# Kernel optimization log

Hardware: AMD Instinct MI355X
Metric: run time of the kernel (lower is better)

The kernel has to match this reference:

```python
import jax, jax.numpy as jnp
import numpy as np

T, H, I, E, K = 1024, 2880, 2880, 16, 4
ALPHA = 1.702   # gemm1_alpha
LIMIT = 7.0     # swiglu_limit (gemm1_clamp_limit)


def setup_inputs() -> dict:
    key = jax.random.key(0)
    ks = jax.random.split(key, 9)
    s = 0.02  # init scale to keep activations sane
    return {
        "hidden_states": jax.random.normal(ks[0], (T, H), jnp.float32),
        "router_w": jax.random.normal(ks[1], (E, H), jnp.float32) * s,
        "router_b": jax.random.normal(ks[2], (E,), jnp.float32) * s,
        "w_gate": jax.random.normal(ks[3], (E, H, I), jnp.float32) * s,
        "b_gate": jax.random.normal(ks[4], (E, I), jnp.float32) * s,
        "w_up": jax.random.normal(ks[5], (E, H, I), jnp.float32) * s,
        "b_up": jax.random.normal(ks[6], (E, I), jnp.float32) * s,
        "w_down": jax.random.normal(ks[7], (E, I, H), jnp.float32) * s,
        "b_down": jax.random.normal(ks[8], (E, H), jnp.float32) * s,
    }


def reference(hidden_states, router_w, router_b, w_gate, b_gate, w_up, b_up, w_down, b_down):
    x = hidden_states  # [T, H]
    # Router: ReplicatedLinear(hidden_size, num_experts, bias=True)
    logits = x @ router_w.T + router_b            # [T, E]
    # TopK(top_k=K, renormalize=True): softmax -> top-k -> renormalize
    probs = jax.nn.softmax(logits, axis=-1)
    top_w, top_i = jax.lax.top_k(probs, K)        # [T, K]
    top_w = top_w / jnp.sum(top_w, axis=-1, keepdims=True)
    # combine weights scattered back to [T, E] (rows sum to 1)
    comb = jnp.sum(jax.nn.one_hot(top_i, E, dtype=x.dtype) * top_w[..., None], axis=1)
    # Expert grouped GEMM (dense over experts; combine weights zero out unused)
    g = jnp.einsum('th,ehi->eti', x, w_gate) + b_gate[:, None, :]   # [E, T, I]
    u = jnp.einsum('th,ehi->eti', x, w_up) + b_up[:, None, :]       # [E, T, I]
    # gpt-oss clamped swiglu: gate clamp max, up clamp both sides
    g = jnp.minimum(g, LIMIT)
    u = jnp.clip(u, -LIMIT, LIMIT)
    act = (u + 1.0) * (g * jax.nn.sigmoid(g * ALPHA))               # [E, T, I]
    y = jnp.einsum('eti,eih->eth', act, w_down) + b_down[:, None, :]  # [E, T, H]
    out = jnp.einsum('te,eth->th', comb, y)                          # [T, H]
    return out
```

## Files before the change

kernel.cpp:

```cpp
#include <hip/hip_runtime.h>
#include <stdint.h>

#define T_TOK 1024
#define HD 2880
#define ID 2880
#define NE 16
#define NTOP 4

#define BM 128
#define BN 64
#define BK 64
#define NKT (HD / BK)
#define NIB (ID / BN)
#define NMB (T_TOK / BM)
#define NB1 (NE * NIB * NMB)

typedef short bf16x8 __attribute__((ext_vector_type(8)));
typedef float f32x4 __attribute__((ext_vector_type(4)));

__device__ __forceinline__ uint4 pack8f(const float* v) {
    union { __bf16 b[8]; uint4 q; } p;
#pragma unroll
    for (int j = 0; j < 8; j++) p.b[j] = (__bf16)v[j];
    return p.q;
}
__device__ __forceinline__ unsigned short bf16bits(float f) {
    union { __bf16 b[2]; unsigned short u[2]; } p;
    p.b[0] = (__bf16)f;
    return p.u[0];
}

__global__ __launch_bounds__(256) void k_init(float* __restrict__ out, int* __restrict__ cnt) {
    int i = blockIdx.x * 256 + threadIdx.x;
    ((float4*)out)[i] = make_float4(0.f, 0.f, 0.f, 0.f);
    if (blockIdx.x == 0 && threadIdx.x < NE) cnt[threadIdx.x] = 0;
}

__global__ __launch_bounds__(256) void k_router(
    const float* __restrict__ x, const float* __restrict__ rw, const float* __restrict__ rb,
    float* __restrict__ topw, int* __restrict__ cnt, int* __restrict__ list)
{
    const int t = blockIdx.x;
    const int tid = threadIdx.x;
    float acc[NE];
#pragma unroll
    for (int e = 0; e < NE; e++) acc[e] = 0.f;
    for (int c = tid; c < HD; c += 256) {
        float xv = x[(size_t)t * HD + c];
#pragma unroll
        for (int e = 0; e < NE; e++) acc[e] += xv * rw[(size_t)e * HD + c];
    }
    __shared__ float red[4][NE];
    const int lane = tid & 63, wv = tid >> 6;
#pragma unroll
    for (int e = 0; e < NE; e++) {
        float v = acc[e];
#pragma unroll
        for (int off = 32; off > 0; off >>= 1) v += __shfl_down(v, off, 64);
        if (lane == 0) red[wv][e] = v;
    }
    __syncthreads();
    if (tid == 0) {
        float p[NE];
        float mx = -1e30f;
        for (int e = 0; e < NE; e++) {
            float v = red[0][e] + red[1][e] + red[2][e] + red[3][e] + rb[e];
            p[e] = v; mx = fmaxf(mx, v);
        }
        for (int e = 0; e < NE; e++) p[e] = expf(p[e] - mx);
        int sel[NTOP]; float pw[NTOP]; float ssum = 0.f;
        for (int k = 0; k < NTOP; k++) {
            float best = -1.f; int bi = 0;
            for (int e = 0; e < NE; e++)
                if (p[e] > best) { best = p[e]; bi = e; }
            sel[k] = bi; pw[k] = best; ssum += best; p[bi] = -2.f;
        }
        for (int k = 0; k < NTOP; k++) {
            topw[t * NTOP + k] = pw[k] / ssum;
            int e = sel[k];
            int pos = atomicAdd(&cnt[e], 1);
            list[e * T_TOK + pos] = t * NTOP + k;
        }
    }
}

__global__ void k_scan(const int* __restrict__ cnt, int* __restrict__ offs) {
    if (threadIdx.x == 0 && blockIdx.x == 0) {
        int s = 0;
        for (int e = 0; e < NE; e++) { offs[e] = s; s += cnt[e]; }
        offs[NE] = s;
    }
}

__global__ __launch_bounds__(512) void k_gemm1(
    const float* __restrict__ x,
    const float* __restrict__ wg, const float* __restrict__ bg,
    const float* __restrict__ wu, const float* __restrict__ bu,
    const int* __restrict__ cnt, const int* __restrict__ offs,
    const int* __restrict__ list,
    unsigned short* __restrict__ act)
{
    const int lin = blockIdx.x;
    const int logical = (lin & 7) * (NB1 / 8) + (lin >> 3);
    const int mblk = logical & 7;
    const int iblk = (logical >> 3) % NIB;
    const int e = logical / (NIB * NMB);

    const int count = cnt[e];
    const int m0 = mblk * BM;
    if (m0 >= count) return;
    const int mcount = min(BM, count - m0);
    const int i0 = iblk * BN;
    const int tid = threadIdx.x;

    __shared__ char sA[2][BM * BK * 2];
    __shared__ char sG[2][BN * BK * 2];
    __shared__ char sU[2][BN * BK * 2];
    __shared__ int lidx[BM];

    if (tid < BM) lidx[tid] = list[e * T_TOK + m0 + min(tid, mcount - 1)];
    __syncthreads();

    const int ar = tid >> 2, acg = tid & 3;
    const float* asrc = x + (size_t)(lidx[ar] >> 2) * HD + acg * 16;

    const int wtid = tid & 255;
    const int wc = wtid & 63, whg = wtid >> 6;
    const float* wsrc = (tid < 256 ? wg : wu) + ((size_t)e * HD + whg * 16) * ID + i0 + wc;
    char* const wdst0 = (tid < 256 ? sG[0] : sU[0]);
    char* const wdst1 = (tid < 256 ? sG[1] : sU[1]);

    const int lane = tid & 63, wid = tid >> 6;
    const int wm = wid >> 1, wn = wid & 1;
    const int lr = lane & 15, lk = lane >> 4;

    float4 ra[4];
    float rwv[16];

#define LOAD1(kt) do { \
        const float* s_ = asrc + (kt) * BK; \
        ra[0] = ((const float4*)s_)[0]; ra[1] = ((const float4*)s_)[1]; \
        ra[2] = ((const float4*)s_)[2]; ra[3] = ((const float4*)s_)[3]; \
        const float* w_ = wsrc + (size_t)(kt) * BK * ID; \
        _Pragma("unroll") \
        for (int j_ = 0; j_ < 16; j_++) rwv[j_] = w_[(size_t)j_ * ID]; \
    } while (0)

#define STORE1(buf) do { \
        float v_[16]; \
        _Pragma("unroll") \
        for (int p_ = 0; p_ < 4; p_++) { \
            v_[p_ * 4 + 0] = ra[p_].x; v_[p_ * 4 + 1] = ra[p_].y; \
            v_[p_ * 4 + 2] = ra[p_].z; v_[p_ * 4 + 3] = ra[p_].w; \
        } \
        *(uint4*)(sA[buf] + ar * 128 + (((acg * 2) ^ (ar & 7)) * 16)) = pack8f(v_); \
        *(uint4*)(sA[buf] + ar * 128 + (((acg * 2 + 1) ^ (ar & 7)) * 16)) = pack8f(v_ + 8); \
        char* wd_ = (buf) ? wdst1 : wdst0; \
        *(uint4*)(wd_ + wc * 128 + (((whg * 2) ^ (wc & 7)) * 16)) = pack8f(rwv); \
        *(uint4*)(wd_ + wc * 128 + (((whg * 2 + 1) ^ (wc & 7)) * 16)) = pack8f(rwv + 8); \
    } while (0)

    f32x4 accG[2][2], accU[2][2];
#pragma unroll
    for (int mb = 0; mb < 2; mb++)
#pragma unroll
        for (int cb = 0; cb < 2; cb++) {
            accG[mb][cb] = (f32x4){0.f, 0.f, 0.f, 0.f};
            accU[mb][cb] = (f32x4){0.f, 0.f, 0.f, 0.f};
        }

    LOAD1(0);
    STORE1(0);
    __syncthreads();

    for (int kt = 0; kt < NKT; kt++) {
        const int cur = kt & 1;
        const bool more = (kt + 1 < NKT);
        if (more) LOAD1(kt + 1);
        const char* cA = sA[cur];
        const char* cG = sG[cur];
        const char* cU = sU[cur];
#pragma unroll
        for (int ks = 0; ks < 2; ks++) {
            const int s = ks * 4 + lk;
            bf16x8 af[2], gf[2], uf[2];
#pragma unroll
            for (int mb = 0; mb < 2; mb++) {
                int rr = wm * 32 + mb * 16 + lr;
                af[mb] = *(const bf16x8*)(cA + rr * 128 + ((s ^ (rr & 7)) * 16));
            }
#pragma unroll
            for (int cb = 0; cb < 2; cb++) {
                int ii = wn * 32 + cb * 16 + lr;
                gf[cb] = *(const bf16x8*)(cG + ii * 128 + ((s ^ (ii & 7)) * 16));
                uf[cb] = *(const bf16x8*)(cU + ii * 128 + ((s ^ (ii & 7)) * 16));
            }
#pragma unroll
            for (int mb = 0; mb < 2; mb++)
#pragma unroll
                for (int cb = 0; cb < 2; cb++) {
                    accG[mb][cb] = __builtin_amdgcn_mfma_f32_16x16x32_bf16(af[mb], gf[cb], accG[mb][cb], 0, 0, 0);
                    accU[mb][cb] = __builtin_amdgcn_mfma_f32_16x16x32_bf16(af[mb], uf[cb], accU[mb][cb], 0, 0, 0);
                }
        }
        if (more) STORE1(cur ^ 1);
        __syncthreads();
    }
#undef LOAD1
#undef STORE1

    const int gbase = offs[e] + m0;
#pragma unroll
    for (int mb = 0; mb < 2; mb++)
#pragma unroll
        for (int cb = 0; cb < 2; cb++) {
            const int col = i0 + wn * 32 + cb * 16 + lr;
            const float bgv = bg[e * ID + col];
            const float buv = bu[e * ID + col];
#pragma unroll
            for (int q = 0; q < 4; q++) {
                const int r = wm * 32 + mb * 16 + lk * 4 + q;
                if (r < mcount) {
                    float gv = fminf(accG[mb][cb][q] + bgv, 7.0f);
                    float uv = fminf(fmaxf(accU[mb][cb][q] + buv, -7.0f), 7.0f);
                    float av = (uv + 1.0f) * (gv / (1.0f + __expf(-1.702f * gv)));
                    act[(size_t)(gbase + r) * ID + col] = bf16bits(av);
                }
            }
        }
}

__global__ __launch_bounds__(512) void k_gemm2(
    const unsigned short* __restrict__ act,
    const float* __restrict__ wd, const float* __restrict__ bd,
    const float* __restrict__ topw,
    const int* __restrict__ cnt, const int* __restrict__ offs,
    const int* __restrict__ list,
    float* __restrict__ out)
{
    const int lin = blockIdx.x;
    const int logical = (lin & 7) * (NB1 / 8) + (lin >> 3);
    const int mblk = logical & 7;
    const int hblk = (logical >> 3) % NIB;
    const int e = logical / (NIB * NMB);

    const int count = cnt[e];
    const int m0 = mblk * BM;
    if (m0 >= count) return;
    const int mcount = min(BM, count - m0);
    const int h0 = hblk * BN;
    const int tid = threadIdx.x;
    const int gbase = offs[e] + m0;

    __shared__ char sA[2][BM * BK * 2];
    __shared__ char sW[2][BN * BK * 2];
    __shared__ int lidx[BM];

    if (tid < BM) lidx[tid] = list[e * T_TOK + m0 + min(tid, mcount - 1)];
    __syncthreads();

    const int ar = tid >> 2, acg = tid & 3;
    const int arow = gbase + min(ar, mcount - 1);
    const unsigned short* asrc = act + (size_t)arow * ID + acg * 16;

    const int wc = tid & 63, whg = tid >> 6;
    const float* wsrc = wd + (size_t)e * ID * HD + (size_t)(whg * 8) * HD + h0 + wc;

    const int lane = tid & 63, wid = tid >> 6;
    const int wm = wid >> 1, wn = wid & 1;
    const int lr = lane & 15, lk = lane >> 4;

    uint4 ra0, ra1;
    float rwv[8];

#define LOAD2(kt) do { \
        const uint4* s_ = (const uint4*)(asrc + (kt) * BK); \
        ra0 = s_[0]; ra1 = s_[1]; \
        const float* w_ = wsrc + (size_t)(kt) * BK * HD; \
        _Pragma("unroll") \
        for (int j_ = 0; j_ < 8; j_++) rwv[j_] = w_[(size_t)j_ * HD]; \
    } while (0)

#define STORE2(buf) do { \
        *(uint4*)(sA[buf] + ar * 128 + (((acg * 2) ^ (ar & 7)) * 16)) = ra0; \
        *(uint4*)(sA[buf] + ar * 128 + (((acg * 2 + 1) ^ (ar & 7)) * 16)) = ra1; \
        *(uint4*)(sW[buf] + wc * 128 + ((whg ^ (wc & 7)) * 16)) = pack8f(rwv); \
    } while (0)

    f32x4 acc[2][2];
#pragma unroll
    for (int mb = 0; mb < 2; mb++)
#pragma unroll
        for (int cb = 0; cb < 2; cb++) acc[mb][cb] = (f32x4){0.f, 0.f, 0.f, 0.f};

    LOAD2(0);
    STORE2(0);
    __syncthreads();

    for (int kt = 0; kt < NKT; kt++) {
        const int cur = kt & 1;
        const bool more = (kt + 1 < NKT);
        if (more) LOAD2(kt + 1);
        const char* cA = sA[cur];
        const char* cW = sW[cur];
#pragma unroll
        for (int ks = 0; ks < 2; ks++) {
            const int s = ks * 4 + lk;
            bf16x8 af[2], wf[2];
#pragma unroll
            for (int mb = 0; mb < 2; mb++) {
                int rr = wm * 32 + mb * 16 + lr;
                af[mb] = *(const bf16x8*)(cA + rr * 128 + ((s ^ (rr & 7)) * 16));
            }
#pragma unroll
            for (int cb = 0; cb < 2; cb++) {
                int ii = wn * 32 + cb * 16 + lr;
                wf[cb] = *(const bf16x8*)(cW + ii * 128 + ((s ^ (ii & 7)) * 16));
            }
#pragma unroll
            for (int mb = 0; mb < 2; mb++)
#pragma unroll
                for (int cb = 0; cb < 2; cb++)
                    acc[mb][cb] = __builtin_amdgcn_mfma_f32_16x16x32_bf16(af[mb], wf[cb], acc[mb][cb], 0, 0, 0);
        }
        if (more) STORE2(cur ^ 1);
        __syncthreads();
    }
#undef LOAD2
#undef STORE2

#pragma unroll
    for (int mb = 0; mb < 2; mb++)
#pragma unroll
        for (int cb = 0; cb < 2; cb++) {
            const int col = h0 + wn * 32 + cb * 16 + lr;
            const float bdv = bd[e * HD + col];
#pragma unroll
            for (int q = 0; q < 4; q++) {
                const int r = wm * 32 + mb * 16 + lk * 4 + q;
                if (r < mcount) {
                    int idx = lidx[r];
                    float w = topw[idx];
                    atomicAdd(&out[(size_t)(idx >> 2) * HD + col], w * (acc[mb][cb][q] + bdv));
                }
            }
        }
}

extern "C" void kernel_launch(void* const* d_in, const int* in_sizes, int n_in,
                              void* d_out, int out_size, void* d_ws, size_t ws_size,
                              hipStream_t stream)
{
    const float* x  = (const float*)d_in[0];
    const float* rw = (const float*)d_in[1];
    const float* rb = (const float*)d_in[2];
    const float* wg = (const float*)d_in[3];
    const float* bg = (const float*)d_in[4];
    const float* wu = (const float*)d_in[5];
    const float* bu = (const float*)d_in[6];
    const float* wd = (const float*)d_in[7];
    const float* bd = (const float*)d_in[8];
    float* out = (float*)d_out;

    char* ws = (char*)d_ws;
    int*   cnt  = (int*)(ws + 0);
    int*   offs = (int*)(ws + 256);
    float* topw = (float*)(ws + 1024);
    int*   list = (int*)(ws + 32768);
    unsigned short* act = (unsigned short*)(ws + 131072);

    hipLaunchKernelGGL(k_init, dim3(T_TOK * HD / 1024), dim3(256), 0, stream, out, cnt);
    hipLaunchKernelGGL(k_router, dim3(T_TOK), dim3(256), 0, stream, x, rw, rb, topw, cnt, list);
    hipLaunchKernelGGL(k_scan, dim3(1), dim3(64), 0, stream, cnt, offs);
    hipLaunchKernelGGL(k_gemm1, dim3(NB1), dim3(512), 0, stream,
                       x, wg, bg, wu, bu, cnt, offs, list, act);
    hipLaunchKernelGGL(k_gemm2, dim3(NB1), dim3(512), 0, stream,
                       act, wd, bd, topw, cnt, offs, list, out);
}
```

Before: 1.082 ms.

## Pre-convert x to bf16 and load A fragments directly from global memory

```diff
diff --git a/kernel.cpp b/kernel.cpp
--- a/kernel.cpp
+++ b/kernel.cpp
@@ -36,6 +36,16 @@
     if (blockIdx.x == 0 && threadIdx.x < NE) cnt[threadIdx.x] = 0;
 }
 
+__global__ __launch_bounds__(256) void k_xbf(const float* __restrict__ x, unsigned short* __restrict__ xbf) {
+    const size_t i = (size_t)blockIdx.x * 256 + threadIdx.x;
+    float v[8];
+    float4 a = ((const float4*)x)[i * 2];
+    float4 b = ((const float4*)x)[i * 2 + 1];
+    v[0] = a.x; v[1] = a.y; v[2] = a.z; v[3] = a.w;
+    v[4] = b.x; v[5] = b.y; v[6] = b.z; v[7] = b.w;
+    ((uint4*)xbf)[i] = pack8f(v);
+}
+
 __global__ __launch_bounds__(256) void k_router(
     const float* __restrict__ x, const float* __restrict__ rw, const float* __restrict__ rb,
     float* __restrict__ topw, int* __restrict__ cnt, int* __restrict__ list)
@@ -92,8 +102,8 @@
     }
 }
 
-__global__ __launch_bounds__(512) void k_gemm1(
-    const float* __restrict__ x,
+__global__ __launch_bounds__(512, 6) void k_gemm1(
+    const unsigned short* __restrict__ xbf,
     const float* __restrict__ wg, const float* __restrict__ bg,
     const float* __restrict__ wu, const float* __restrict__ bu,
     const int* __restrict__ cnt, const int* __restrict__ offs,
@@ -113,52 +123,35 @@
     const int i0 = iblk * BN;
     const int tid = threadIdx.x;
 
-    __shared__ char sA[2][BM * BK * 2];
     __shared__ char sG[2][BN * BK * 2];
     __shared__ char sU[2][BN * BK * 2];
     __shared__ int lidx[BM];
 
     if (tid < BM) lidx[tid] = list[e * T_TOK + m0 + min(tid, mcount - 1)];
-    __syncthreads();
-
-    const int ar = tid >> 2, acg = tid & 3;
-    const float* asrc = x + (size_t)(lidx[ar] >> 2) * HD + acg * 16;
 
     const int wtid = tid & 255;
     const int wc = wtid & 63, whg = wtid >> 6;
     const float* wsrc = (tid < 256 ? wg : wu) + ((size_t)e * HD + whg * 16) * ID + i0 + wc;
-    char* const wdst0 = (tid < 256 ? sG[0] : sU[0]);
-    char* const wdst1 = (tid < 256 ? sG[1] : sU[1]);
+    char* const wb0 = (tid < 256 ? sG[0] : sU[0]);
+    char* const wb1 = (tid < 256 ? sG[1] : sU[1]);
 
     const int lane = tid & 63, wid = tid >> 6;
     const int wm = wid >> 1, wn = wid & 1;
     const int lr = lane & 15, lk = lane >> 4;
 
-    float4 ra[4];
     float rwv[16];
-
-#define LOAD1(kt) do { \
-        const float* s_ = asrc + (kt) * BK; \
-        ra[0] = ((const float4*)s_)[0]; ra[1] = ((const float4*)s_)[1]; \
-        ra[2] = ((const float4*)s_)[2]; ra[3] = ((const float4*)s_)[3]; \
-        const float* w_ = wsrc + (size_t)(kt) * BK * ID; \
-        _Pragma("unroll") \
-        for (int j_ = 0; j_ < 16; j_++) rwv[j_] = w_[(size_t)j_ * ID]; \
-    } while (0)
-
-#define STORE1(buf) do { \
-        float v_[16]; \
-        _Pragma("unroll") \
-        for (int p_ = 0; p_ < 4; p_++) { \
-            v_[p_ * 4 + 0] = ra[p_].x; v_[p_ * 4 + 1] = ra[p_].y; \
-            v_[p_ * 4 + 2] = ra[p_].z; v_[p_ * 4 + 3] = ra[p_].w; \
-        } \
-        *(uint4*)(sA[buf] + ar * 128 + (((acg * 2) ^ (ar & 7)) * 16)) = pack8f(v_); \
-        *(uint4*)(sA[buf] + ar * 128 + (((acg * 2 + 1) ^ (ar & 7)) * 16)) = pack8f(v_ + 8); \
-        char* wd_ = (buf) ? wdst1 : wdst0; \
-        *(uint4*)(wd_ + wc * 128 + (((whg * 2) ^ (wc & 7)) * 16)) = pack8f(rwv); \
-        *(uint4*)(wd_ + wc * 128 + (((whg * 2 + 1) ^ (wc & 7)) * 16)) = pack8f(rwv + 8); \
-    } while (0)
+#define LOADW1(kt_) { _Pragma("unroll") \
+        for (int j_ = 0; j_ < 16; j_++) rwv[j_] = wsrc[(size_t)((kt_) * BK + j_) * ID]; }
+#define STOREW1(dst_) { \
+        *(uint4*)((dst_) + wc * 128 + (((whg * 2) ^ (wc & 7)) * 16)) = pack8f(rwv); \
+        *(uint4*)((dst_) + wc * 128 + (((whg * 2 + 1) ^ (wc & 7)) * 16)) = pack8f(rwv + 8); }
+
+    LOADW1(0);
+    __syncthreads();
+    const unsigned short* arow0 = xbf + (size_t)(lidx[wm * 32 + lr] >> 2) * HD;
+    const unsigned short* arow1 = xbf + (size_t)(lidx[wm * 32 + 16 + lr] >> 2) * HD;
+    STOREW1(wb0);
+    __syncthreads();
 
     f32x4 accG[2][2], accU[2][2];
 #pragma unroll
@@ -169,45 +162,37 @@
             accU[mb][cb] = (f32x4){0.f, 0.f, 0.f, 0.f};
         }
 
-    LOAD1(0);
-    STORE1(0);
-    __syncthreads();
-
     for (int kt = 0; kt < NKT; kt++) {
-        const int cur = kt & 1;
         const bool more = (kt + 1 < NKT);
-        if (more) LOAD1(kt + 1);
-        const char* cA = sA[cur];
-        const char* cG = sG[cur];
-        const char* cU = sU[cur];
+        if (more) LOADW1(kt + 1);
+        bf16x8 af[2][2];
+#pragma unroll
+        for (int ks = 0; ks < 2; ks++) {
+            const int koff = kt * BK + (ks * 4 + lk) * 8;
+            af[ks][0] = *(const bf16x8*)(arow0 + koff);
+            af[ks][1] = *(const bf16x8*)(arow1 + koff);
+        }
+        const char* cG = sG[kt & 1];
+        const char* cU = sU[kt & 1];
 #pragma unroll
         for (int ks = 0; ks < 2; ks++) {
             const int s = ks * 4 + lk;
-            bf16x8 af[2], gf[2], uf[2];
-#pragma unroll
-            for (int mb = 0; mb < 2; mb++) {
-                int rr = wm * 32 + mb * 16 + lr;
-                af[mb] = *(const bf16x8*)(cA + rr * 128 + ((s ^ (rr & 7)) * 16));
+#pragma unroll
+            for (int cb = 0; cb < 2; cb++) {
+                const int ii = wn * 32 + cb * 16 + lr;
+                bf16x8 gf = *(const bf16x8*)(cG + ii * 128 + ((s ^ (ii & 7)) * 16));
+                accG[0][cb] = __builtin_amdgcn_mfma_f32_16x16x32_bf16(af[ks][0], gf, accG[0][cb], 0, 0, 0);
+                accG[1][cb] = __builtin_amdgcn_mfma_f32_16x16x32_bf16(af[ks][1], gf, accG[1][cb], 0, 0, 0);
+                bf16x8 uf = *(const bf16x8*)(cU + ii * 128 + ((s ^ (ii & 7)) * 16));
+                accU[0][cb] = __builtin_amdgcn_mfma_f32_16x16x32_bf16(af[ks][0], uf, accU[0][cb], 0, 0, 0);
+                accU[1][cb] = __builtin_amdgcn_mfma_f32_16x16x32_bf16(af[ks][1], uf, accU[1][cb], 0, 0, 0);
             }
-#pragma unroll
-            for (int cb = 0; cb < 2; cb++) {
-                int ii = wn * 32 + cb * 16 + lr;
-                gf[cb] = *(const bf16x8*)(cG + ii * 128 + ((s ^ (ii & 7)) * 16));
-                uf[cb] = *(const bf16x8*)(cU + ii * 128 + ((s ^ (ii & 7)) * 16));
-            }
-#pragma unroll
-            for (int mb = 0; mb < 2; mb++)
-#pragma unroll
-                for (int cb = 0; cb < 2; cb++) {
-                    accG[mb][cb] = __builtin_amdgcn_mfma_f32_16x16x32_bf16(af[mb], gf[cb], accG[mb][cb], 0, 0, 0);
-                    accU[mb][cb] = __builtin_amdgcn_mfma_f32_16x16x32_bf16(af[mb], uf[cb], accU[mb][cb], 0, 0, 0);
-                }
-        }
-        if (more) STORE1(cur ^ 1);
+        }
+        if (more) { STOREW1(((kt & 1) ? wb0 : wb1)); }
         __syncthreads();
     }
-#undef LOAD1
-#undef STORE1
+#undef LOADW1
+#undef STOREW1
 
     const int gbase = offs[e] + m0;
 #pragma unroll
@@ -230,7 +215,7 @@
         }
 }
 
-__global__ __launch_bounds__(512) void k_gemm2(
+__global__ __launch_bounds__(512, 8) void k_gemm2(
     const unsigned short* __restrict__ act,
     const float* __restrict__ wd, const float* __restrict__ bd,
     const float* __restrict__ topw,
@@ -252,16 +237,10 @@
     const int tid = threadIdx.x;
     const int gbase = offs[e] + m0;
 
-    __shared__ char sA[2][BM * BK * 2];
     __shared__ char sW[2][BN * BK * 2];
     __shared__ int lidx[BM];
 
     if (tid < BM) lidx[tid] = list[e * T_TOK + m0 + min(tid, mcount - 1)];
-    __syncthreads();
-
-    const int ar = tid >> 2, acg = tid & 3;
-    const int arow = gbase + min(ar, mcount - 1);
-    const unsigned short* asrc = act + (size_t)arow * ID + acg * 16;
 
     const int wc = tid & 63, whg = tid >> 6;
     const float* wsrc = wd + (size_t)e * ID * HD + (size_t)(whg * 8) * HD + h0 + wc;
@@ -270,22 +249,20 @@
     const int wm = wid >> 1, wn = wid & 1;
     const int lr = lane & 15, lk = lane >> 4;
 
-    uint4 ra0, ra1;
     float rwv[8];
-
-#define LOAD2(kt) do { \
-        const uint4* s_ = (const uint4*)(asrc + (kt) * BK); \
-        ra0 = s_[0]; ra1 = s_[1]; \
-        const float* w_ = wsrc + (size_t)(kt) * BK * HD; \
-        _Pragma("unroll") \
-        for (int j_ = 0; j_ < 8; j_++) rwv[j_] = w_[(size_t)j_ * HD]; \
-    } while (0)
-
-#define STORE2(buf) do { \
-        *(uint4*)(sA[buf] + ar * 128 + (((acg * 2) ^ (ar & 7)) * 16)) = ra0; \
-        *(uint4*)(sA[buf] + ar * 128 + (((acg * 2 + 1) ^ (ar & 7)) * 16)) = ra1; \
-        *(uint4*)(sW[buf] + wc * 128 + ((whg ^ (wc & 7)) * 16)) = pack8f(rwv); \
-    } while (0)
+#define LOADW2(kt_) { _Pragma("unroll") \
+        for (int j_ = 0; j_ < 8; j_++) rwv[j_] = wsrc[(size_t)((kt_) * BK + j_) * HD]; }
+#define STOREW2(dst_) { \
+        *(uint4*)((dst_) + wc * 128 + ((whg ^ (wc & 7)) * 16)) = pack8f(rwv); }
+
+    LOADW2(0);
+    __syncthreads();
+    const int r0 = gbase + min(wm * 32 + lr, mcount - 1);
+    const int r1 = gbase + min(wm * 32 + 16 + lr, mcount - 1);
+    const unsigned short* arow0 = act + (size_t)r0 * ID;
+    const unsigned short* arow1 = act + (size_t)r1 * ID;
+    STOREW2(sW[0]);
+    __syncthreads();
 
     f32x4 acc[2][2];
 #pragma unroll
@@ -293,41 +270,33 @@
 #pragma unroll
         for (int cb = 0; cb < 2; cb++) acc[mb][cb] = (f32x4){0.f, 0.f, 0.f, 0.f};
 
-    LOAD2(0);
-    STORE2(0);
-    __syncthreads();
-
     for (int kt = 0; kt < NKT; kt++) {
-        const int cur = kt & 1;
         const bool more = (kt + 1 < NKT);
-        if (more) LOAD2(kt + 1);
-        const char* cA = sA[cur];
-        const char* cW = sW[cur];
+        if (more) LOADW2(kt + 1);
+        bf16x8 af[2][2];
+#pragma unroll
+        for (int ks = 0; ks < 2; ks++) {
+            const int koff = kt * BK + (ks * 4 + lk) * 8;
+            af[ks][0] = *(const bf16x8*)(arow0 + koff);
+            af[ks][1] = *(const bf16x8*)(arow1 + koff);
+        }
+        const char* cW = sW[kt & 1];
 #pragma unroll
         for (int ks = 0; ks < 2; ks++) {
             const int s = ks * 4 + lk;
-            bf16x8 af[2], wf[2];
-#pragma unroll
-            for (int mb = 0; mb < 2; mb++) {
-                int rr = wm * 32 + mb * 16 + lr;
-                af[mb] = *(const bf16x8*)(cA + rr * 128 + ((s ^ (rr & 7)) * 16));
+#pragma unroll
+            for (int cb = 0; cb < 2; cb++) {
+                const int ii = wn * 32 + cb * 16 + lr;
+                bf16x8 wf = *(const bf16x8*)(cW + ii * 128 + ((s ^ (ii & 7)) * 16));
+                acc[0][cb] = __builtin_amdgcn_mfma_f32_16x16x32_bf16(af[ks][0], wf, acc[0][cb], 0, 0, 0);
+                acc[1][cb] = __builtin_amdgcn_mfma_f32_16x16x32_bf16(af[ks][1], wf, acc[1][cb], 0, 0, 0);
             }
-#pragma unroll
-            for (int cb = 0; cb < 2; cb++) {
-                int ii = wn * 32 + cb * 16 + lr;
-                wf[cb] = *(const bf16x8*)(cW + ii * 128 + ((s ^ (ii & 7)) * 16));
-            }
-#pragma unroll
-            for (int mb = 0; mb < 2; mb++)
-#pragma unroll
-                for (int cb = 0; cb < 2; cb++)
-                    acc[mb][cb] = __builtin_amdgcn_mfma_f32_16x16x32_bf16(af[mb], wf[cb], acc[mb][cb], 0, 0, 0);
-        }
-        if (more) STORE2(cur ^ 1);
+        }
+        if (more) { STOREW2(((kt & 1) ? sW[0] : sW[1])); }
         __syncthreads();
     }
-#undef LOAD2
-#undef STORE2
+#undef LOADW2
+#undef STOREW2
 
 #pragma unroll
     for (int mb = 0; mb < 2; mb++)
@@ -368,12 +337,14 @@
     float* topw = (float*)(ws + 1024);
     int*   list = (int*)(ws + 32768);
     unsigned short* act = (unsigned short*)(ws + 131072);
+    unsigned short* xbf = (unsigned short*)(ws + 131072 + (size_t)4096 * ID * 2);
 
     hipLaunchKernelGGL(k_init, dim3(T_TOK * HD / 1024), dim3(256), 0, stream, out, cnt);
+    hipLaunchKernelGGL(k_xbf, dim3(T_TOK * HD / (256 * 8)), dim3(256), 0, stream, x, xbf);
     hipLaunchKernelGGL(k_router, dim3(T_TOK), dim3(256), 0, stream, x, rw, rb, topw, cnt, list);
     hipLaunchKernelGGL(k_scan, dim3(1), dim3(64), 0, stream, cnt, offs);
     hipLaunchKernelGGL(k_gemm1, dim3(NB1), dim3(512), 0, stream,
-                       x, wg, bg, wu, bu, cnt, offs, list, act);
+                       xbf, wg, bg, wu, bu, cnt, offs, list, act);
     hipLaunchKernelGGL(k_gemm2, dim3(NB1), dim3(512), 0, stream,
                        act, wd, bd, topw, cnt, offs, list, out);
 }
```

Measured after the change: 1.798 ms. 1.66x slower.
